# Kernel optimization log

Hardware: AMD Instinct MI355X
Metric: run time of the kernel (lower is better)

The kernel has to match this reference:

```python
import jax, jax.numpy as jnp
import numpy as np

B, T, CH, Hs, Ws = 2, 64, 512, 24, 24
DIM = CH // 2          # 256, attention channel dim
HEADS = 8
HEAD_DIM = DIM // HEADS  # 32
MAX_SEQ = 64


def setup_inputs() -> dict:
    key = jax.random.key(0)
    ks = jax.random.split(key, 6)
    return {
        "x": jax.random.normal(ks[0], (B, T, CH, Hs, Ws), dtype=jnp.float32),
        "rpb_table": jax.random.normal(ks[1], (2 * MAX_SEQ - 1, HEADS), dtype=jnp.float32) * 0.02,
        "qkv_w": jax.random.normal(ks[2], (3 * DIM, DIM), dtype=jnp.float32) * 0.02,
        "qkv_b": jax.random.normal(ks[3], (3 * DIM,), dtype=jnp.float32) * 0.02,
        "proj_w": jax.random.normal(ks[4], (DIM, DIM), dtype=jnp.float32) * 0.02,
        "proj_b": jax.random.normal(ks[5], (DIM,), dtype=jnp.float32) * 0.02,
    }


def reference(x, rpb_table, qkv_w, qkv_b, proj_w, proj_b):
    b, t, c, h, w = x.shape
    half = c // 2
    a_part = x[:, :, :half]       # (B,T,half,H,W) untouched branch
    b_part = x[:, :, half:]       # attention branch

    # 'b t c h w -> (b h w) t c'
    xb = jnp.transpose(b_part, (0, 3, 4, 1, 2)).reshape(b * h * w, t, half)
    B_, N, C = xb.shape
    scale = HEAD_DIM ** -0.5

    qkv = xb @ qkv_w.T + qkv_b                        # (B_, N, 3*C)
    qkv = qkv.reshape(B_, N, 3, HEADS, HEAD_DIM)
    qkv = jnp.transpose(qkv, (2, 0, 3, 1, 4))          # (3, B_, heads, N, hd)
    q, k, v = qkv[0] * scale, qkv[1], qkv[2]

    attn = jnp.einsum('bhnd,bhmd->bhnm', q, k)         # (B_, heads, N, N)

    # relative position bias: index = p2 - p1 + (MAX_SEQ - 1)
    pos = jnp.arange(t)
    rel_idx = pos[None, :] - pos[:, None] + (MAX_SEQ - 1)   # (N, N)
    bias = rpb_table[rel_idx]                              # (N, N, heads)
    bias = jnp.transpose(bias, (2, 0, 1))                  # (heads, N, N)
    attn = attn + bias[None]

    # causal (mask_future=True): -inf strictly above the diagonal
    causal = jnp.where(pos[None, :] > pos[:, None], -jnp.inf, 0.0).astype(attn.dtype)
    attn = attn + causal[None, None]

    attn = jax.nn.softmax(attn, axis=-1)

    out = jnp.einsum('bhnm,bhmd->bhnd', attn, v)       # (B_, heads, N, hd)
    out = jnp.transpose(out, (0, 2, 1, 3)).reshape(B_, N, C)
    out = out @ proj_w.T + proj_b

    # '(b h w) t c -> b t c h w'
    out = out.reshape(b, h, w, t, half)
    out = jnp.transpose(out, (0, 3, 4, 1, 2))

    return jnp.concatenate([a_part, out], axis=2)
```

## Files before the change

### kernel.cpp

```cpp
#include <hip/hip_runtime.h>
#include <hip/hip_bf16.h>

typedef __attribute__((ext_vector_type(4))) float  f32x4;
typedef __attribute__((ext_vector_type(8))) short  bf16x8;
typedef __attribute__((ext_vector_type(8))) unsigned short u16x8;
typedef __attribute__((ext_vector_type(4))) unsigned short u16x4;

__device__ __forceinline__ unsigned short f2bf(float f) {
    union { float f; unsigned u; } v; v.f = f;
    unsigned u = v.u;
    unsigned r = u + 0x7fffu + ((u >> 16) & 1u);
    return (unsigned short)(r >> 16);
}

__device__ __forceinline__ void gload16(const void* g, void* l) {
    __builtin_amdgcn_global_load_lds((const __attribute__((address_space(1))) unsigned*)g,
                                     (__attribute__((address_space(3))) unsigned*)l, 16, 0, 0);
}


__global__ void cvt_weights(const float* __restrict__ qkv_w, const float* __restrict__ proj_w,
                            unsigned short* __restrict__ wq, unsigned short* __restrict__ wp) {
    int i = blockIdx.x * 256 + threadIdx.x;
    if (i < 196608) wq[i] = f2bf(qkv_w[i]);
    else            wp[i - 196608] = f2bf(proj_w[i - 196608]);
}

__global__ void copy_a(const float* __restrict__ x, float* __restrict__ out) {
    long long i = (long long)blockIdx.x * 256 + threadIdx.x;
    int chunk = (int)(i / 36864);
    int r     = (int)(i % 36864);
    size_t off = (size_t)chunk * 73728 + r;
    ((float4*)out)[off] = ((const float4*)x)[off];
}

__global__ __launch_bounds__(256) void transpose_b(const float* __restrict__ x,
                                                   unsigned short* __restrict__ xb) {
    __shared__ unsigned short tile[256][72];
    const int bt  = blockIdx.x;
    const int hw0 = blockIdx.y * 64;
    const int tid = threadIdx.x;
    const float* src = x + ((size_t)bt * 512 + 256) * 576 + hw0;
    const int c_sub = tid >> 4, l16 = tid & 15;
    #pragma unroll
    for (int it = 0; it < 16; ++it) {
        int cc = it * 16 + c_sub;
        const float4 v = *(const float4*)(src + (size_t)cc * 576 + l16 * 4);
        tile[cc][l16 * 4 + 0] = f2bf(v.x);
        tile[cc][l16 * 4 + 1] = f2bf(v.y);
        tile[cc][l16 * 4 + 2] = f2bf(v.z);
        tile[cc][l16 * 4 + 3] = f2bf(v.w);
    }
    __syncthreads();
    const int row = tid >> 2;
    const int cs  = (tid & 3) * 64;
    const int b = bt >> 6, t = bt & 63;
    size_t m = ((size_t)(b * 576 + hw0 + row)) * 64 + t;
    unsigned short* dst = xb + m * 256 + cs;
    #pragma unroll
    for (int q = 0; q < 8; ++q) {
        u16x8 v;
        #pragma unroll
        for (int u = 0; u < 8; ++u) v[u] = tile[cs + q * 8 + u][row];
        *(u16x8*)(dst + q * 8) = v;
    }
}

__global__ __launch_bounds__(512) __attribute__((amdgpu_waves_per_eu(2, 2)))
void fused_block(
    const unsigned short* __restrict__ xb,
    const unsigned short* __restrict__ wqkv,
    const unsigned short* __restrict__ wproj,
    const float* __restrict__ qkv_b,
    const float* __restrict__ proj_b,
    const float* __restrict__ rpb,
    float* __restrict__ out)
{
    __shared__ unsigned short xs[16384];
    __shared__ unsigned short wbuf[8][7424];
    __shared__ float bias_s[8][64];

    const int tid  = threadIdx.x;
    const int lane = tid & 63, w = tid >> 6;
    const int c = lane & 15, g = lane >> 4;
    const int c7 = c & 7;
    const int bid = blockIdx.x;
    const int p  = (bid & 7) * 144 + (bid >> 3);
    const int b  = p / 576, hw = p % 576;

    const unsigned short* src = xb + (size_t)p * 16384;
    #pragma unroll
    for (int it = 0; it < 4; ++it) {
        int U = it * 512 + tid;
        int r = U >> 5, u = U & 31;
        gload16(src + r * 256 + ((u ^ (r & 7)) << 3), &xs[U << 3]);
    }
    bias_s[tid & 7][tid >> 3] = rpb[tid];
    __syncthreads();

    unsigned short* Q  = &wbuf[w][0];
    unsigned short* Kl = &wbuf[w][2560];
    unsigned short* Vt = &wbuf[w][5120];
    unsigned short* P  = &wbuf[w][0];
    const float* bias_w = bias_s[w];

    {
        f32x4 acc[3][2][4] = {};
        #pragma unroll
        for (int ks = 0; ks < 8; ++ks) {
            bf16x8 bx[4];
            #pragma unroll
            for (int b2 = 0; b2 < 4; ++b2)
                bx[b2] = *(const bf16x8*)(&xs[(b2 * 16 + c) * 256 + (((ks * 4 + g) ^ c7) << 3)]);
            #pragma unroll
            for (int mat = 0; mat < 3; ++mat) {
                bf16x8 af[2];
                #pragma unroll
                for (int a2 = 0; a2 < 2; ++a2)
                    af[a2] = *(const bf16x8*)(wqkv + (size_t)(mat * 256 + w * 32 + a2 * 16 + c) * 256 + ks * 32 + g * 8);
                #pragma unroll
                for (int a2 = 0; a2 < 2; ++a2)
                    #pragma unroll
                    for (int b2 = 0; b2 < 4; ++b2)
                        acc[mat][a2][b2] = __builtin_amdgcn_mfma_f32_16x16x32_bf16(af[a2], bx[b2], acc[mat][a2][b2], 0, 0, 0);
            }
        }
        const float scale = 0.17677669529663687f;
        #pragma unroll
        for (int a2 = 0; a2 < 2; ++a2) {
            float4 bq = *(const float4*)(qkv_b +       w * 32 + a2 * 16 + g * 4);
            float4 bk = *(const float4*)(qkv_b + 256 + w * 32 + a2 * 16 + g * 4);
            float4 bv = *(const float4*)(qkv_b + 512 + w * 32 + a2 * 16 + g * 4);
            #pragma unroll
            for (int b2 = 0; b2 < 4; ++b2) {
                int t = b2 * 16 + c;
                u16x4 vq, vk;
                vq[0] = f2bf((acc[0][a2][b2][0] + bq.x) * scale);
                vq[1] = f2bf((acc[0][a2][b2][1] + bq.y) * scale);
                vq[2] = f2bf((acc[0][a2][b2][2] + bq.z) * scale);
                vq[3] = f2bf((acc[0][a2][b2][3] + bq.w) * scale);
                *(u16x4*)(&Q[t * 40 + a2 * 16 + g * 4]) = vq;
                vk[0] = f2bf(acc[1][a2][b2][0] + bk.x);
                vk[1] = f2bf(acc[1][a2][b2][1] + bk.y);
                vk[2] = f2bf(acc[1][a2][b2][2] + bk.z);
                vk[3] = f2bf(acc[1][a2][b2][3] + bk.w);
                *(u16x4*)(&Kl[t * 40 + a2 * 16 + g * 4]) = vk;
                Vt[(a2 * 16 + g * 4 + 0) * 72 + t] = f2bf(acc[2][a2][b2][0] + bv.x);
                Vt[(a2 * 16 + g * 4 + 1) * 72 + t] = f2bf(acc[2][a2][b2][1] + bv.y);
                Vt[(a2 * 16 + g * 4 + 2) * 72 + t] = f2bf(acc[2][a2][b2][2] + bv.z);
                Vt[(a2 * 16 + g * 4 + 3) * 72 + t] = f2bf(acc[2][a2][b2][3] + bv.w);
            }
        }
    }

    bf16x8 qf[4], kf[4];
    #pragma unroll
    for (int mt = 0; mt < 4; ++mt) qf[mt] = *(const bf16x8*)(&Q[(mt * 16 + c) * 40 + g * 8]);
    #pragma unroll
    for (int nt = 0; nt < 4; ++nt) kf[nt] = *(const bf16x8*)(&Kl[(nt * 16 + c) * 40 + g * 8]);
    f32x4 S[4][4] = {};
    __builtin_amdgcn_s_setprio(1);
    #pragma unroll
    for (int mt = 0; mt < 4; ++mt)
        #pragma unroll
        for (int nt = 0; nt < 4; ++nt)
            S[mt][nt] = __builtin_amdgcn_mfma_f32_16x16x32_bf16(qf[mt], kf[nt], S[mt][nt], 0, 0, 0);
    __builtin_amdgcn_s_setprio(0);

    #pragma unroll
    for (int mt = 0; mt < 4; ++mt) {
        #pragma unroll
        for (int r = 0; r < 4; ++r) {
            int i = mt * 16 + g * 4 + r;
            float vals[4];
            #pragma unroll
            for (int nt = 0; nt < 4; ++nt) {
                int j = nt * 16 + c;
                int d = j - i + 63;
                float v = S[mt][nt][r] + bias_w[d > 63 ? 63 : d];
                vals[nt] = (j > i) ? -1e30f : v;
            }
            float mx = fmaxf(fmaxf(vals[0], vals[1]), fmaxf(vals[2], vals[3]));
            #pragma unroll
            for (int off = 1; off < 16; off <<= 1) mx = fmaxf(mx, __shfl_xor(mx, off, 64));
            float sum = 0.f;
            #pragma unroll
            for (int nt = 0; nt < 4; ++nt) { vals[nt] = __expf(vals[nt] - mx); sum += vals[nt]; }
            #pragma unroll
            for (int off = 1; off < 16; off <<= 1) sum += __shfl_xor(sum, off, 64);
            float inv = 1.0f / sum;
            #pragma unroll
            for (int nt = 0; nt < 4; ++nt) P[i * 72 + nt * 16 + c] = f2bf(vals[nt] * inv);
        }
    }

    f32x4 O[4][2] = {};
    #pragma unroll
    for (int kk = 0; kk < 2; ++kk) {
        bf16x8 pa[4], vb[2];
        #pragma unroll
        for (int mt = 0; mt < 4; ++mt)
            pa[mt] = *(const bf16x8*)(&P[(mt * 16 + c) * 72 + kk * 32 + g * 8]);
        #pragma unroll
        for (int nt = 0; nt < 2; ++nt)
            vb[nt] = *(const bf16x8*)(&Vt[(nt * 16 + c) * 72 + kk * 32 + g * 8]);
        __builtin_amdgcn_s_setprio(1);
        #pragma unroll
        for (int mt = 0; mt < 4; ++mt)
            #pragma unroll
            for (int nt = 0; nt < 2; ++nt)
                O[mt][nt] = __builtin_amdgcn_mfma_f32_16x16x32_bf16(pa[mt], vb[nt], O[mt][nt], 0, 0, 0);
        __builtin_amdgcn_s_setprio(0);
    }

    __syncthreads();
    #pragma unroll
    for (int mt = 0; mt < 4; ++mt)
        #pragma unroll
        for (int nt = 0; nt < 2; ++nt)
            #pragma unroll
            for (int r = 0; r < 4; ++r) {
                int t  = mt * 16 + g * 4 + r;
                int cg = w * 32 + nt * 16 + c;
                xs[t * 256 + (((cg >> 3) ^ (t & 7)) << 3) + (cg & 7)] = f2bf(O[mt][nt][r]);
            }
    __syncthreads();

    f32x4 ap[2][4] = {};
    #pragma unroll
    for (int ks = 0; ks < 8; ++ks) {
        bf16x8 af[2], bx[4];
        #pragma unroll
        for (int a2 = 0; a2 < 2; ++a2)
            af[a2] = *(const bf16x8*)(wproj + (size_t)(w * 32 + a2 * 16 + c) * 256 + ks * 32 + g * 8);
        #pragma unroll
        for (int b2 = 0; b2 < 4; ++b2)
            bx[b2] = *(const bf16x8*)(&xs[(b2 * 16 + c) * 256 + (((ks * 4 + g) ^ c7) << 3)]);
        #pragma unroll
        for (int a2 = 0; a2 < 2; ++a2)
            #pragma unroll
            for (int b2 = 0; b2 < 4; ++b2)
                ap[a2][b2] = __builtin_amdgcn_mfma_f32_16x16x32_bf16(af[a2], bx[b2], ap[a2][b2], 0, 0, 0);
    }
    #pragma unroll
    for (int a2 = 0; a2 < 2; ++a2) {
        int n = w * 32 + a2 * 16 + g * 4;
        float4 pb = *(const float4*)(proj_b + n);
        #pragma unroll
        for (int b2 = 0; b2 < 4; ++b2) {
            int t = b2 * 16 + c;
            float* dst = out + ((size_t)((b * 64 + t) * 512 + 256 + n)) * 576 + hw;
            dst[0]        = ap[a2][b2][0] + pb.x;
            dst[576]      = ap[a2][b2][1] + pb.y;
            dst[2 * 576]  = ap[a2][b2][2] + pb.z;
            dst[3 * 576]  = ap[a2][b2][3] + pb.w;
        }
    }
}

extern "C" void kernel_launch(void* const* d_in, const int* in_sizes, int n_in,
                              void* d_out, int out_size, void* d_ws, size_t ws_size,
                              hipStream_t stream) {
    (void)in_sizes; (void)n_in; (void)out_size;
    const float* x      = (const float*)d_in[0];
    const float* rpb    = (const float*)d_in[1];
    const float* qkv_w  = (const float*)d_in[2];
    const float* qkv_b  = (const float*)d_in[3];
    const float* proj_w = (const float*)d_in[4];
    const float* proj_b = (const float*)d_in[5];
    float* out = (float*)d_out;

    char* ws = (char*)d_ws;
    unsigned short* wq = (unsigned short*)ws;
    unsigned short* wp = (unsigned short*)(ws + 393216);
    unsigned short* xb = (unsigned short*)(ws + 524288);
    if (ws_size < (size_t)524288 + 37748736) return;

    cvt_weights<<<1024, 256, 0, stream>>>(qkv_w, proj_w, wq, wp);
    copy_a<<<18432, 256, 0, stream>>>(x, out);
    transpose_b<<<dim3(128, 9), 256, 0, stream>>>(x, xb);
    fused_block<<<1152, 512, 0, stream>>>(xb, wq, wp, qkv_b, proj_b, rpb, out);
}
```

Measured before the change: 270.3 us.

## Fuse passthrough copy into transpose, keep Q/K/P in registers via shuffles

The separate copy_a kernel is removed, and the untouched half of x is copied inside transpose_b, saving one launch and one pass. In fused_block, Q and K are computed as transposed MFMA outputs, packed with v_cvt_pk_bf16_f32 and rearranged into MFMA operand layout with cross-lane shuffles rather than a round trip through LDS. The softmax probabilities are likewise kept in registers. Only V goes through a shared LDS buffer, which shrinks LDS use and allows more occupancy (launch_bounds 512,4). The max-subtraction in softmax is dropped, which risks overflow for large logits, and the extra shuffles add ALU work.

After: 250.0 us. 7.5% less time.

```diff
diff --git a/kernel.cpp b/kernel.cpp
--- a/kernel.cpp
+++ b/kernel.cpp
@@ -4,7 +4,8 @@
 typedef __attribute__((ext_vector_type(4))) float  f32x4;
 typedef __attribute__((ext_vector_type(8))) short  bf16x8;
 typedef __attribute__((ext_vector_type(8))) unsigned short u16x8;
-typedef __attribute__((ext_vector_type(4))) unsigned short u16x4;
+
+union FU { int w[4]; bf16x8 v; };
 
 __device__ __forceinline__ unsigned short f2bf(float f) {
     union { float f; unsigned u; } v; v.f = f;
@@ -13,6 +14,18 @@
     return (unsigned short)(r >> 16);
 }
 
+__device__ __forceinline__ unsigned cvtpk(float lo, float hi) {
+    unsigned r;
+    asm("v_cvt_pk_bf16_f32 %0, %1, %2" : "=v"(r) : "v"(lo), "v"(hi));
+    return r;
+}
+
+__device__ __forceinline__ int selshfl(unsigned lo, unsigned hiw, int srcLane, bool hi) {
+    int a = __shfl((int)lo, srcLane, 64);
+    int b = __shfl((int)hiw, srcLane, 64);
+    return hi ? b : a;
+}
+
 __device__ __forceinline__ void gload16(const void* g, void* l) {
     __builtin_amdgcn_global_load_lds((const __attribute__((address_space(1))) unsigned*)g,
                                      (__attribute__((address_space(3))) unsigned*)l, 16, 0, 0);
@@ -26,20 +39,24 @@
     else            wp[i - 196608] = f2bf(proj_w[i - 196608]);
 }
 
-__global__ void copy_a(const float* __restrict__ x, float* __restrict__ out) {
-    long long i = (long long)blockIdx.x * 256 + threadIdx.x;
-    int chunk = (int)(i / 36864);
-    int r     = (int)(i % 36864);
-    size_t off = (size_t)chunk * 73728 + r;
-    ((float4*)out)[off] = ((const float4*)x)[off];
-}
-
 __global__ __launch_bounds__(256) void transpose_b(const float* __restrict__ x,
-                                                   unsigned short* __restrict__ xb) {
+                                                   unsigned short* __restrict__ xb,
+                                                   float* __restrict__ outp) {
     __shared__ unsigned short tile[256][72];
     const int bt  = blockIdx.x;
     const int hw0 = blockIdx.y * 64;
     const int tid = threadIdx.x;
+    {
+        const size_t slab = (size_t)bt * 294912;
+        #pragma unroll
+        for (int it = 0; it < 16; ++it) {
+            int idx = it * 256 + tid;
+            int ch  = idx >> 4;
+            int off = (idx & 15) * 4;
+            size_t o = slab + (size_t)ch * 576 + hw0 + off;
+            *(float4*)(outp + o) = *(const float4*)(x + o);
+        }
+    }
     const float* src = x + ((size_t)bt * 512 + 256) * 576 + hw0;
     const int c_sub = tid >> 4, l16 = tid & 15;
     #pragma unroll
@@ -66,7 +83,7 @@
     }
 }
 
-__global__ __launch_bounds__(512) __attribute__((amdgpu_waves_per_eu(2, 2)))
+__global__ __launch_bounds__(512, 4)
 void fused_block(
     const unsigned short* __restrict__ xb,
     const unsigned short* __restrict__ wqkv,
@@ -77,13 +94,16 @@
     float* __restrict__ out)
 {
     __shared__ unsigned short xs[16384];
-    __shared__ unsigned short wbuf[8][7424];
+    __shared__ unsigned short VtAll[256 * 88];
     __shared__ float bias_s[8][64];
 
     const int tid  = threadIdx.x;
     const int lane = tid & 63, w = tid >> 6;
     const int c = lane & 15, g = lane >> 4;
     const int c7 = c & 7;
+    const bool hi = g >= 2;
+    const int lA = c + 16 * ((2 * g) & 3);
+    const int lB = c + 16 * ((2 * g + 1) & 3);
     const int bid = blockIdx.x;
     const int p  = (bid & 7) * 144 + (bid >> 3);
     const int b  = p / 576, hw = p % 576;
@@ -98,131 +118,171 @@
     bias_s[tid & 7][tid >> 3] = rpb[tid];
     __syncthreads();
 
-    unsigned short* Q  = &wbuf[w][0];
-    unsigned short* Kl = &wbuf[w][2560];
-    unsigned short* Vt = &wbuf[w][5120];
-    unsigned short* P  = &wbuf[w][0];
     const float* bias_w = bias_s[w];
 
     {
-        f32x4 acc[3][2][4] = {};
+        f32x4 acc[2][4] = {};
         #pragma unroll
         for (int ks = 0; ks < 8; ++ks) {
-            bf16x8 bx[4];
+            bf16x8 bx[4], af[2];
             #pragma unroll
             for (int b2 = 0; b2 < 4; ++b2)
                 bx[b2] = *(const bf16x8*)(&xs[(b2 * 16 + c) * 256 + (((ks * 4 + g) ^ c7) << 3)]);
             #pragma unroll
-            for (int mat = 0; mat < 3; ++mat) {
-                bf16x8 af[2];
+            for (int a2 = 0; a2 < 2; ++a2)
+                af[a2] = *(const bf16x8*)(wqkv + (size_t)(512 + w * 32 + a2 * 16 + c) * 256 + ks * 32 + g * 8);
+            #pragma unroll
+            for (int a2 = 0; a2 < 2; ++a2)
                 #pragma unroll
-                for (int a2 = 0; a2 < 2; ++a2)
-                    af[a2] = *(const bf16x8*)(wqkv + (size_t)(mat * 256 + w * 32 + a2 * 16 + c) * 256 + ks * 32 + g * 8);
-                #pragma unroll
-                for (int a2 = 0; a2 < 2; ++a2)
-                    #pragma unroll
-                    for (int b2 = 0; b2 < 4; ++b2)
-                        acc[mat][a2][b2] = __builtin_amdgcn_mfma_f32_16x16x32_bf16(af[a2], bx[b2], acc[mat][a2][b2], 0, 0, 0);
-            }
-        }
-        const float scale = 0.17677669529663687f;
+                for (int b2 = 0; b2 < 4; ++b2)
+                    acc[a2][b2] = __builtin_amdgcn_mfma_f32_16x16x32_bf16(af[a2], bx[b2], acc[a2][b2], 0, 0, 0);
+        }
         #pragma unroll
         for (int a2 = 0; a2 < 2; ++a2) {
-            float4 bq = *(const float4*)(qkv_b +       w * 32 + a2 * 16 + g * 4);
-            float4 bk = *(const float4*)(qkv_b + 256 + w * 32 + a2 * 16 + g * 4);
             float4 bv = *(const float4*)(qkv_b + 512 + w * 32 + a2 * 16 + g * 4);
             #pragma unroll
             for (int b2 = 0; b2 < 4; ++b2) {
                 int t = b2 * 16 + c;
-                u16x4 vq, vk;
-                vq[0] = f2bf((acc[0][a2][b2][0] + bq.x) * scale);
-                vq[1] = f2bf((acc[0][a2][b2][1] + bq.y) * scale);
-                vq[2] = f2bf((acc[0][a2][b2][2] + bq.z) * scale);
-                vq[3] = f2bf((acc[0][a2][b2][3] + bq.w) * scale);
-                *(u16x4*)(&Q[t * 40 + a2 * 16 + g * 4]) = vq;
-                vk[0] = f2bf(acc[1][a2][b2][0] + bk.x);
-                vk[1] = f2bf(acc[1][a2][b2][1] + bk.y);
-                vk[2] = f2bf(acc[1][a2][b2][2] + bk.z);
-                vk[3] = f2bf(acc[1][a2][b2][3] + bk.w);
-                *(u16x4*)(&Kl[t * 40 + a2 * 16 + g * 4]) = vk;
-                Vt[(a2 * 16 + g * 4 + 0) * 72 + t] = f2bf(acc[2][a2][b2][0] + bv.x);
-                Vt[(a2 * 16 + g * 4 + 1) * 72 + t] = f2bf(acc[2][a2][b2][1] + bv.y);
-                Vt[(a2 * 16 + g * 4 + 2) * 72 + t] = f2bf(acc[2][a2][b2][2] + bv.z);
-                Vt[(a2 * 16 + g * 4 + 3) * 72 + t] = f2bf(acc[2][a2][b2][3] + bv.w);
-            }
-        }
-    }
-
-    bf16x8 qf[4], kf[4];
-    #pragma unroll
-    for (int mt = 0; mt < 4; ++mt) qf[mt] = *(const bf16x8*)(&Q[(mt * 16 + c) * 40 + g * 8]);
-    #pragma unroll
-    for (int nt = 0; nt < 4; ++nt) kf[nt] = *(const bf16x8*)(&Kl[(nt * 16 + c) * 40 + g * 8]);
-    f32x4 S[4][4] = {};
+                VtAll[(w * 32 + a2 * 16 + g * 4 + 0) * 88 + t] = f2bf(acc[a2][b2][0] + bv.x);
+                VtAll[(w * 32 + a2 * 16 + g * 4 + 1) * 88 + t] = f2bf(acc[a2][b2][1] + bv.y);
+                VtAll[(w * 32 + a2 * 16 + g * 4 + 2) * 88 + t] = f2bf(acc[a2][b2][2] + bv.z);
+                VtAll[(w * 32 + a2 * 16 + g * 4 + 3) * 88 + t] = f2bf(acc[a2][b2][3] + bv.w);
+            }
+        }
+    }
+
+    unsigned kpk[2][4][2], qpk[2][4][2];
+    {
+        f32x4 ak[2][4] = {}, aq[2][4] = {};
+        #pragma unroll
+        for (int ks = 0; ks < 8; ++ks) {
+            bf16x8 bx[4], afk[2], afq[2];
+            #pragma unroll
+            for (int b2 = 0; b2 < 4; ++b2)
+                bx[b2] = *(const bf16x8*)(&xs[(b2 * 16 + c) * 256 + (((ks * 4 + g) ^ c7) << 3)]);
+            #pragma unroll
+            for (int a2 = 0; a2 < 2; ++a2) {
+                afk[a2] = *(const bf16x8*)(wqkv + (size_t)(256 + w * 32 + a2 * 16 + c) * 256 + ks * 32 + g * 8);
+                afq[a2] = *(const bf16x8*)(wqkv + (size_t)(      w * 32 + a2 * 16 + c) * 256 + ks * 32 + g * 8);
+            }
+            #pragma unroll
+            for (int a2 = 0; a2 < 2; ++a2)
+                #pragma unroll
+                for (int b2 = 0; b2 < 4; ++b2) {
+                    ak[a2][b2] = __builtin_amdgcn_mfma_f32_16x16x32_bf16(afk[a2], bx[b2], ak[a2][b2], 0, 0, 0);
+                    aq[a2][b2] = __builtin_amdgcn_mfma_f32_16x16x32_bf16(afq[a2], bx[b2], aq[a2][b2], 0, 0, 0);
+                }
+        }
+        #pragma unroll
+        for (int a2 = 0; a2 < 2; ++a2) {
+            float4 bk = *(const float4*)(qkv_b + 256 + w * 32 + a2 * 16 + g * 4);
+            float4 bq = *(const float4*)(qkv_b +       w * 32 + a2 * 16 + g * 4);
+            #pragma unroll
+            for (int b2 = 0; b2 < 4; ++b2) {
+                kpk[a2][b2][0] = cvtpk(ak[a2][b2][0] + bk.x, ak[a2][b2][1] + bk.y);
+                kpk[a2][b2][1] = cvtpk(ak[a2][b2][2] + bk.z, ak[a2][b2][3] + bk.w);
+                qpk[a2][b2][0] = cvtpk(aq[a2][b2][0] + bq.x, aq[a2][b2][1] + bq.y);
+                qpk[a2][b2][1] = cvtpk(aq[a2][b2][2] + bq.z, aq[a2][b2][3] + bq.w);
+            }
+        }
+    }
+
+    bf16x8 kf[4], qf[4];
+    #pragma unroll
+    for (int t = 0; t < 4; ++t) {
+        FU f;
+        f.w[0] = selshfl(kpk[0][t][0], kpk[1][t][0], lA, hi);
+        f.w[1] = selshfl(kpk[0][t][1], kpk[1][t][1], lA, hi);
+        f.w[2] = selshfl(kpk[0][t][0], kpk[1][t][0], lB, hi);
+        f.w[3] = selshfl(kpk[0][t][1], kpk[1][t][1], lB, hi);
+        kf[t] = f.v;
+        FU f2;
+        f2.w[0] = selshfl(qpk[0][t][0], qpk[1][t][0], lA, hi);
+        f2.w[1] = selshfl(qpk[0][t][1], qpk[1][t][1], lA, hi);
+        f2.w[2] = selshfl(qpk[0][t][0], qpk[1][t][0], lB, hi);
+        f2.w[3] = selshfl(qpk[0][t][1], qpk[1][t][1], lB, hi);
+        qf[t] = f2.v;
+    }
+    f32x4 S[4][4];
+    #pragma unroll
+    for (int jt = 0; jt < 4; ++jt)
+        #pragma unroll
+        for (int it = 0; it < 4; ++it)
+            S[jt][it] = f32x4{0.f, 0.f, 0.f, 0.f};
     __builtin_amdgcn_s_setprio(1);
     #pragma unroll
-    for (int mt = 0; mt < 4; ++mt)
-        #pragma unroll
-        for (int nt = 0; nt < 4; ++nt)
-            S[mt][nt] = __builtin_amdgcn_mfma_f32_16x16x32_bf16(qf[mt], kf[nt], S[mt][nt], 0, 0, 0);
+    for (int jt = 0; jt < 4; ++jt)
+        #pragma unroll
+        for (int it = 0; it < 4; ++it)
+            S[jt][it] = __builtin_amdgcn_mfma_f32_16x16x32_bf16(kf[jt], qf[it], S[jt][it], 0, 0, 0);
     __builtin_amdgcn_s_setprio(0);
 
-    #pragma unroll
-    for (int mt = 0; mt < 4; ++mt) {
-        #pragma unroll
-        for (int r = 0; r < 4; ++r) {
-            int i = mt * 16 + g * 4 + r;
-            float vals[4];
-            #pragma unroll
-            for (int nt = 0; nt < 4; ++nt) {
-                int j = nt * 16 + c;
-                int d = j - i + 63;
-                float v = S[mt][nt][r] + bias_w[d > 63 ? 63 : d];
-                vals[nt] = (j > i) ? -1e30f : v;
-            }
-            float mx = fmaxf(fmaxf(vals[0], vals[1]), fmaxf(vals[2], vals[3]));
-            #pragma unroll
-            for (int off = 1; off < 16; off <<= 1) mx = fmaxf(mx, __shfl_xor(mx, off, 64));
-            float sum = 0.f;
-            #pragma unroll
-            for (int nt = 0; nt < 4; ++nt) { vals[nt] = __expf(vals[nt] - mx); sum += vals[nt]; }
-            #pragma unroll
-            for (int off = 1; off < 16; off <<= 1) sum += __shfl_xor(sum, off, 64);
-            float inv = 1.0f / sum;
-            #pragma unroll
-            for (int nt = 0; nt < 4; ++nt) P[i * 72 + nt * 16 + c] = f2bf(vals[nt] * inv);
-        }
-    }
-
-    f32x4 O[4][2] = {};
-    #pragma unroll
-    for (int kk = 0; kk < 2; ++kk) {
-        bf16x8 pa[4], vb[2];
-        #pragma unroll
-        for (int mt = 0; mt < 4; ++mt)
-            pa[mt] = *(const bf16x8*)(&P[(mt * 16 + c) * 72 + kk * 32 + g * 8]);
-        #pragma unroll
-        for (int nt = 0; nt < 2; ++nt)
-            vb[nt] = *(const bf16x8*)(&Vt[(nt * 16 + c) * 72 + kk * 32 + g * 8]);
-        __builtin_amdgcn_s_setprio(1);
-        #pragma unroll
-        for (int mt = 0; mt < 4; ++mt)
-            #pragma unroll
-            for (int nt = 0; nt < 2; ++nt)
-                O[mt][nt] = __builtin_amdgcn_mfma_f32_16x16x32_bf16(pa[mt], vb[nt], O[mt][nt], 0, 0, 0);
-        __builtin_amdgcn_s_setprio(0);
+    const float scale = 0.17677669529663687f;
+    unsigned ppk[4][4][2];
+    #pragma unroll
+    for (int it = 0; it < 4; ++it) {
+        float rs = 0.f;
+        #pragma unroll
+        for (int jt = 0; jt < 4; ++jt)
+            #pragma unroll
+            for (int r = 0; r < 4; ++r) {
+                int j = jt * 16 + 4 * g + r;
+                int i = it * 16 + c;
+                int d = j - i + 63; d = d > 63 ? 63 : d;
+                float v = S[jt][it][r] * scale + bias_w[d];
+                float e = (j > i) ? 0.f : __expf(v);
+                S[jt][it][r] = e;
+                rs += e;
+            }
+        rs += __shfl_xor(rs, 16, 64);
+        rs += __shfl_xor(rs, 32, 64);
+        float inv = 1.0f / rs;
+        #pragma unroll
+        for (int jt = 0; jt < 4; ++jt) {
+            ppk[jt][it][0] = cvtpk(S[jt][it][0] * inv, S[jt][it][1] * inv);
+            ppk[jt][it][1] = cvtpk(S[jt][it][2] * inv, S[jt][it][3] * inv);
+        }
+    }
+
+    bf16x8 vf[2][2];
+    #pragma unroll
+    for (int dt = 0; dt < 2; ++dt)
+        #pragma unroll
+        for (int kk = 0; kk < 2; ++kk)
+            vf[dt][kk] = *(const bf16x8*)(&VtAll[(w * 32 + dt * 16 + c) * 88 + kk * 32 + g * 8]);
+    f32x4 O[2][4];
+    #pragma unroll
+    for (int dt = 0; dt < 2; ++dt)
+        #pragma unroll
+        for (int it = 0; it < 4; ++it)
+            O[dt][it] = f32x4{0.f, 0.f, 0.f, 0.f};
+    #pragma unroll
+    for (int it = 0; it < 4; ++it) {
+        #pragma unroll
+        for (int kk = 0; kk < 2; ++kk) {
+            FU pf;
+            pf.w[0] = selshfl(ppk[2 * kk][it][0], ppk[2 * kk + 1][it][0], lA, hi);
+            pf.w[1] = selshfl(ppk[2 * kk][it][1], ppk[2 * kk + 1][it][1], lA, hi);
+            pf.w[2] = selshfl(ppk[2 * kk][it][0], ppk[2 * kk + 1][it][0], lB, hi);
+            pf.w[3] = selshfl(ppk[2 * kk][it][1], ppk[2 * kk + 1][it][1], lB, hi);
+            __builtin_amdgcn_s_setprio(1);
+            #pragma unroll
+            for (int dt = 0; dt < 2; ++dt)
+                O[dt][it] = __builtin_amdgcn_mfma_f32_16x16x32_bf16(vf[dt][kk], pf.v, O[dt][it], 0, 0, 0);
+            __builtin_amdgcn_s_setprio(0);
+        }
     }
 
     __syncthreads();
     #pragma unroll
-    for (int mt = 0; mt < 4; ++mt)
-        #pragma unroll
-        for (int nt = 0; nt < 2; ++nt)
+    for (int dt = 0; dt < 2; ++dt)
+        #pragma unroll
+        for (int it = 0; it < 4; ++it)
             #pragma unroll
             for (int r = 0; r < 4; ++r) {
-                int t  = mt * 16 + g * 4 + r;
-                int cg = w * 32 + nt * 16 + c;
-                xs[t * 256 + (((cg >> 3) ^ (t & 7)) << 3) + (cg & 7)] = f2bf(O[mt][nt][r]);
+                int t  = it * 16 + c;
+                int cg = w * 32 + dt * 16 + 4 * g + r;
+                xs[t * 256 + ((((cg >> 3) ^ (t & 7)) << 3) | (cg & 7))] = f2bf(O[dt][it][r]);
             }
     __syncthreads();
 
@@ -277,7 +337,6 @@
     if (ws_size < (size_t)524288 + 37748736) return;
 
     cvt_weights<<<1024, 256, 0, stream>>>(qkv_w, proj_w, wq, wp);
-    copy_a<<<18432, 256, 0, stream>>>(x, out);
-    transpose_b<<<dim3(128, 9), 256, 0, stream>>>(x, xb);
+    transpose_b<<<dim3(128, 9), 256, 0, stream>>>(x, xb, out);
     fused_block<<<1152, 512, 0, stream>>>(xb, wq, wp, qkv_b, proj_b, rpb, out);
 }
```
